# Kernel optimization log

Measured on AMD Instinct MI355X. Metric: run time of the kernel, lower is better.

## Reference

```python
import jax, jax.numpy as jnp
import numpy as np

CS = 128            # config.chunk_size
K = 8               # config.k + 1
EPS = 1e-6          # config.eps
L = K * CS          # extended_len = 1024


def setup_inputs() -> dict:
    key = jax.random.key(0)
    k1, k2 = jax.random.split(key)
    B, T, E = 2, 8192, 256
    x = jax.random.normal(k1, (B, T, E), dtype=jnp.float32)
    # xavier_normal_ on [CS, L]: std = sqrt(2 / (fan_in + fan_out))
    std = np.sqrt(2.0 / (CS + L)).astype(np.float32)
    down_proj = jax.random.normal(k2, (CS, L), dtype=jnp.float32) * std
    return {"x": x, "down_proj": down_proj}


def reference(x, down_proj):
    B, T, E = x.shape
    N = T // CS  # T chosen divisible by CS, so the pad branch is a no-op
    chunks = x.reshape(B, N, CS, E)

    # --- per-chunk retrieval scores (vectorized over the causal chunk loop) ---
    cn = chunks / (jnp.linalg.norm(chunks, axis=-1, keepdims=True) + EPS)
    # row-wise cosine sims between every pair of chunks: [B,N,N,CS,CS]
    sims = jnp.einsum('bice,bjde->bijcd', cn, cn)
    scores = sims.max(axis=-1).sum(axis=-1)              # [B,N,N]
    i_idx = jnp.arange(N)
    causal = i_idx[None, :] < i_idx[:, None]             # j < i allowed
    NEG = jnp.asarray(-1e9, x.dtype)
    scores = jnp.where(causal[None], scores, NEG)

    # --- topk selection, weights (num_sel_i = min(i, K-1)) ---
    vals, idx = jax.lax.top_k(scores, K - 1)             # descending, [B,N,K-1]
    num_sel = jnp.minimum(i_idx, K - 1)                  # [N]
    vmin_slot = jnp.clip(num_sel - 1, 0, K - 2)          # last valid slot = min of topk vals
    v_min = jnp.take_along_axis(vals, jnp.broadcast_to(vmin_slot[None, :, None], (B, N, 1)), axis=-1)
    slot = jnp.arange(K - 1)
    valid = slot[None, :] < num_sel[:, None]             # [N,K-1]
    w = jnp.where(valid[None], vals / (v_min + EPS), 0.0)  # [B,N,K-1]

    # --- weighted gather of selected chunks ---
    b_idx = jnp.arange(B)[:, None, None]
    sel = chunks[b_idx, idx]                             # [B,N,K-1,CS,E]
    weighted = sel * w[..., None, None]

    # --- left-pad to L: zeros occupy leftmost slots, then topk-ordered chunks, then cur ---
    shift = jnp.maximum(0, (K - 1) - i_idx)              # [N]
    src = jnp.clip(slot[None, :] - shift[:, None], 0, K - 2)   # [N,K-1]
    n_idx = jnp.arange(N)[None, :, None]
    arranged = weighted[b_idx, n_idx, src[None]]         # [B,N,K-1,CS,E]
    keep = slot[None, :] >= shift[:, None]
    arranged = jnp.where(keep[None, :, :, None, None], arranged, 0.0)

    ext = jnp.concatenate([arranged.reshape(B, N, (K - 1) * CS, E), chunks], axis=2)  # [B,N,L,E]
    # down_proj @ ext + x_chunks, then contract back to [B,T,E]
    out = jnp.einsum('cl,bnle->bnce', down_proj, ext) + chunks
    return out.reshape(B, N * CS, E)
```

## Files before the change

kernel.cpp:

```cpp
#include <hip/hip_runtime.h>
#include <hip/hip_bf16.h>

#define CS     128
#define EDIM   256
#define NBATCH 2
#define TLEN   8192
#define NCHUNK 64
#define LEXT   1024
#define KSEL   7

typedef __attribute__((ext_vector_type(8))) short   short8;
typedef __attribute__((ext_vector_type(4))) float   floatx4;

__device__ inline short bf16_of(float f) {
    __hip_bfloat16 h = __float2bfloat16(f);
    return *(short*)&h;
}
__device__ inline float f_of_bf16(short s) {
    __hip_bfloat16 h = *(__hip_bfloat16*)&s;
    return __bfloat162float(h);
}

__device__ inline void gl_lds16(const void* g, void* l) {
    __builtin_amdgcn_global_load_lds(
        (const __attribute__((address_space(1))) unsigned int*)g,
        (__attribute__((address_space(3))) unsigned int*)l, 16, 0, 0);
}

#define RAW_BAR() asm volatile("s_barrier" ::: "memory")

__global__ __launch_bounds__(256) void prep_kernel(const float* __restrict__ x,
                                                   const float* __restrict__ dp,
                                                   short* __restrict__ cn_hi,
                                                   short* __restrict__ cn_lo,
                                                   short* __restrict__ xt_hi,
                                                   short* __restrict__ dp_hi) {
    const int bx = blockIdx.x;
    if (bx >= 256) {
        int t = (bx - 256) * 256 + threadIdx.x;
#pragma unroll
        for (int u = 0; u < 16; ++u) {
            int idx = (t * 16 + u) * 4;
            float4 v = *(const float4*)(dp + idx);
            *(short4*)(dp_hi + idx) =
                make_short4(bf16_of(v.x), bf16_of(v.y), bf16_of(v.z), bf16_of(v.w));
        }
        return;
    }

    __shared__ float tile[64 * 257];
    const int b = bx >> 7, t0 = (bx & 127) * 64;
    const int tid = threadIdx.x;
    const int r = tid >> 2, q = tid & 3;

    const float* src = x + ((size_t)(b * TLEN + t0 + r)) * EDIM + q * 64;
    float* trow = &tile[r * 257 + q * 64];
    float s = 0.f;
#pragma unroll
    for (int u = 0; u < 16; ++u) {
        float4 v = *(const float4*)(src + u * 4);
        s += v.x * v.x + v.y * v.y + v.z * v.z + v.w * v.w;
        trow[u * 4 + 0] = v.x; trow[u * 4 + 1] = v.y;
        trow[u * 4 + 2] = v.z; trow[u * 4 + 3] = v.w;
    }
    s += __shfl_xor(s, 1);
    s += __shfl_xor(s, 2);
    const float rn = 1.0f / (sqrtf(s) + 1e-6f);

    short* ch = cn_hi + ((size_t)(b * TLEN + t0 + r)) * EDIM + q * 64;
    short* cl = cn_lo + ((size_t)(b * TLEN + t0 + r)) * EDIM + q * 64;
#pragma unroll
    for (int u = 0; u < 16; ++u) {
        short hs[4], ls[4];
#pragma unroll
        for (int k2 = 0; k2 < 4; ++k2) {
            float c = trow[u * 4 + k2] * rn;
            hs[k2] = bf16_of(c);
            ls[k2] = bf16_of(c - f_of_bf16(hs[k2]));
        }
        *(short4*)(ch + u * 4) = make_short4(hs[0], hs[1], hs[2], hs[3]);
        *(short4*)(cl + u * 4) = make_short4(ls[0], ls[1], ls[2], ls[3]);
    }
    __syncthreads();

    const int g16 = tid >> 4, tq = tid & 15;
#pragma unroll
    for (int it = 0; it < 16; ++it) {
        int e = g16 + it * 16;
        short hs2[4];
#pragma unroll
        for (int g = 0; g < 4; ++g)
            hs2[g] = bf16_of(tile[(tq * 4 + g) * 257 + e]);
        *(short4*)(xt_hi + ((size_t)(b * EDIM + e)) * TLEN + t0 + tq * 4)
            = make_short4(hs2[0], hs2[1], hs2[2], hs2[3]);
    }
}

__global__ __launch_bounds__(512) void scores_mfma(const short* __restrict__ cn_hi,
                                                   const short* __restrict__ cn_lo,
                                                   float* __restrict__ scores) {
    __shared__ short tiles[2][4][4096];
    double* red2   = (double*)&tiles[0][0][0];
    float*  redbuf = (float*)&tiles[0][0][8];

    const int p = blockIdx.x, b = blockIdx.y;
    int i = (int)((1.0f + sqrtf(1.0f + 8.0f * (float)p)) * 0.5f);
    while (i * (i - 1) / 2 > p) --i;
    while (i * (i + 1) / 2 <= p) ++i;
    const int j = p - i * (i - 1) / 2;

    const int tid  = threadIdx.x;
    const int w    = tid >> 6, lane = tid & 63;
    const int wr   = w >> 2, wc = w & 3;
    const int quad = lane >> 4, l15 = lane & 15;

    const int tt = w >> 1, hh = w & 1;
    const short* sarr  = (tt & 1) ? cn_lo : cn_hi;
    const size_t sbase = ((size_t)b * TLEN + ((tt >> 1) ? j : i) * CS) * EDIM;
    const int rr  = lane >> 2;
    const int c16 = (lane & 3) * 8;
    const int csw = c16 ^ (((rr >> 1) & 3) * 8);
    const int q8  = (quad ^ ((l15 >> 1) & 3)) * 8;

    auto stage = [&](int ks, int bf) {
        const short* gsrc = sarr + sbase + ks * 32 + csw;
        short* ldst = &tiles[bf][tt][hh * 2048];
#pragma unroll
        for (int t = 0; t < 4; ++t)
            gl_lds16(gsrc + (size_t)(hh * 64 + 16 * t + rr) * EDIM, ldst + t * 512);
    };

    floatx4 acc[4][2];
#pragma unroll
    for (int rt = 0; rt < 4; ++rt)
#pragma unroll
        for (int ct = 0; ct < 2; ++ct) acc[rt][ct] = (floatx4){0.f, 0.f, 0.f, 0.f};

    stage(0, 0);
    int buf = 0;
    for (int ks = 0; ks < 8; ++ks) {
        if (ks < 7) {
            stage(ks + 1, buf ^ 1);
            asm volatile("s_waitcnt vmcnt(4)" ::: "memory");
        } else {
            asm volatile("s_waitcnt vmcnt(0)" ::: "memory");
        }
        RAW_BAR();

        short8 bh[2], bl[2];
#pragma unroll
        for (int ct = 0; ct < 2; ++ct) {
            int r = wc * 32 + ct * 16 + l15;
            bh[ct] = *(const short8*)&tiles[buf][2][r * 32 + q8];
            bl[ct] = *(const short8*)&tiles[buf][3][r * 32 + q8];
        }
        __builtin_amdgcn_s_setprio(1);
#pragma unroll
        for (int rt = 0; rt < 4; ++rt) {
            int r = wr * 64 + rt * 16 + l15;
            short8 ah = *(const short8*)&tiles[buf][0][r * 32 + q8];
            short8 al = *(const short8*)&tiles[buf][1][r * 32 + q8];
#pragma unroll
            for (int ct = 0; ct < 2; ++ct) {
                acc[rt][ct] = __builtin_amdgcn_mfma_f32_16x16x32_bf16(ah, bh[ct], acc[rt][ct], 0, 0, 0);
                acc[rt][ct] = __builtin_amdgcn_mfma_f32_16x16x32_bf16(ah, bl[ct], acc[rt][ct], 0, 0, 0);
                acc[rt][ct] = __builtin_amdgcn_mfma_f32_16x16x32_bf16(al, bh[ct], acc[rt][ct], 0, 0, 0);
            }
        }
        __builtin_amdgcn_s_setprio(0);
        RAW_BAR();
        buf ^= 1;
    }

#pragma unroll
    for (int rt = 0; rt < 4; ++rt) {
        float m[4];
#pragma unroll
        for (int reg = 0; reg < 4; ++reg)
            m[reg] = fmaxf(acc[rt][0][reg], acc[rt][1][reg]);
#pragma unroll
        for (int off = 1; off < 16; off <<= 1)
#pragma unroll
            for (int reg = 0; reg < 4; ++reg) m[reg] = fmaxf(m[reg], __shfl_xor(m[reg], off));
        if (l15 == 0) {
#pragma unroll
            for (int reg = 0; reg < 4; ++reg)
                redbuf[wc * 128 + wr * 64 + rt * 16 + quad * 4 + reg] = m[reg];
        }
    }
    __syncthreads();

    double part = 0.0;
    if (tid < 128)
        part = (double)fmaxf(fmaxf(redbuf[tid], redbuf[128 + tid]),
                             fmaxf(redbuf[256 + tid], redbuf[384 + tid]));
#pragma unroll
    for (int off = 1; off < 64; off <<= 1) part += __shfl_xor(part, off);
    if (lane == 0 && w < 2) red2[w] = part;
    __syncthreads();
    if (tid == 0) scores[(b * NCHUNK + i) * NCHUNK + j] = (float)(red2[0] + red2[1]);
}

__global__ __launch_bounds__(256) void out_mfma(const float* __restrict__ x,
                                                const short* __restrict__ dph,
                                                const short* __restrict__ xth,
                                                const float* __restrict__ scores,
                                                float* __restrict__ out) {
    __shared__ short As[3][2][128 * 32];
    __shared__ short Bs[3][2][64 * 32];
    __shared__ int   slist[8], sslot[8], snum;
    __shared__ float swei[8];

    const int eq = blockIdx.x, n = blockIdx.y, b = blockIdx.z;
    const int e0 = eq * 64;
    const int tid  = threadIdx.x;
    const int w    = tid >> 6, lane = tid & 63;
    const int wr   = w >> 1, wc = w & 1;
    const int quad = lane >> 4, l15 = lane & 15;
    const int rr   = lane >> 2;
    const int c16  = (lane & 3) * 8;
    const int csw  = c16 ^ (((rr >> 1) & 3) * 8);
    const int q8   = (quad ^ ((l15 >> 1) & 3)) * 8;

    if (w == 0) {
        const float* srow = scores + (b * NCHUNK + n) * NCHUNK;
        const int nsel = n < KSEL ? n : KSEL;
        float v = (lane < n) ? srow[lane] : -3.0e38f;
        float vals[KSEL];
        int   idxs[KSEL];
        for (int s2 = 0; s2 < nsel; ++s2) {
            float bv = v; int bi = lane;
#pragma unroll
            for (int off = 1; off < 64; off <<= 1) {
                float ov = __shfl_xor(bv, off);
                int   oi = __shfl_xor(bi, off);
                if (ov > bv || (ov == bv && oi < bi)) { bv = ov; bi = oi; }
            }
            vals[s2] = bv; idxs[s2] = bi;
            if (lane == bi) v = -3.0e38f;
        }
        if (lane == 0) {
            float vmin = (nsel > 0) ? vals[nsel - 1] : 0.0f;
            float inv  = 1.0f / (vmin + 1e-6f);
            int shift  = KSEL - nsel;
            int c = 0;
            for (int s2 = 0; s2 < 8; ++s2) {
                int jj; float ww;
                if (s2 < KSEL) {
                    int tt = s2 - shift;
                    if (tt >= 0) { jj = idxs[tt]; ww = vals[tt] * inv; }
                    else         { jj = -1;       ww = 0.0f; }
                } else { jj = n; ww = 1.0f; }
                if (jj >= 0) { slist[c] = jj; sslot[c] = s2; swei[c] = ww; ++c; }
            }
            snum = c;
        }
    }
    __syncthreads();
    const int NT = snum * 2;

    auto stage = [&](int st, int b3) {
        int sv = st >> 1, kh = st & 1;
        if (w < 2) {
#pragma unroll
            for (int sub = 0; sub < 2; ++sub) {
                const short* gsrc = dph + (size_t)(sslot[sv] * 128 + (kh * 2 + sub) * 32) + csw;
#pragma unroll
                for (int t = 0; t < 4; ++t)
                    gl_lds16(gsrc + (size_t)(w * 64 + t * 16 + rr) * LEXT,
                             &As[b3][sub][(w * 64 + t * 16) * 32]);
            }
        } else {
#pragma unroll
            for (int sub = 0; sub < 2; ++sub) {
                const short* gsrc = xth + ((size_t)(b * EDIM + e0)) * TLEN
                                    + (size_t)(slist[sv] * CS + (kh * 2 + sub) * 32) + csw;
#pragma unroll
                for (int t = 0; t < 2; ++t)
                    gl_lds16(gsrc + (size_t)((w - 2) * 32 + t * 16 + rr) * TLEN,
                             &Bs[b3][sub][((w - 2) * 32 + t * 16) * 32]);
            }
        }
    };

    floatx4 accT[4][2], accP[4][2];
#pragma unroll
    for (int rt = 0; rt < 4; ++rt)
#pragma unroll
        for (int ct = 0; ct < 2; ++ct) accT[rt][ct] = (floatx4){0.f, 0.f, 0.f, 0.f};

    stage(0, 0);
    if (NT > 1) stage(1, 1);
    if (w < 2) asm volatile("s_waitcnt vmcnt(8)" ::: "memory");
    else       asm volatile("s_waitcnt vmcnt(4)" ::: "memory");

    int cur = 0;
    for (int st = 0; st < NT; ++st) {
        RAW_BAR();

        if ((st & 1) == 0) {
#pragma unroll
            for (int rt = 0; rt < 4; ++rt)
#pragma unroll
                for (int ct = 0; ct < 2; ++ct) accP[rt][ct] = (floatx4){0.f, 0.f, 0.f, 0.f};
        }

#pragma unroll
        for (int sub = 0; sub < 2; ++sub) {
            short8 bh[2];
#pragma unroll
            for (int ct = 0; ct < 2; ++ct) {
                int e = wc * 32 + ct * 16 + l15;
                bh[ct] = *(const short8*)&Bs[cur][sub][e * 32 + q8];
            }
            __builtin_amdgcn_s_setprio(1);
#pragma unroll
            for (int rt = 0; rt < 4; ++rt) {
                int r = wr * 64 + rt * 16 + l15;
                short8 ah = *(const short8*)&As[cur][sub][r * 32 + q8];
#pragma unroll
                for (int ct = 0; ct < 2; ++ct)
                    accP[rt][ct] = __builtin_amdgcn_mfma_f32_16x16x32_bf16(ah, bh[ct], accP[rt][ct], 0, 0, 0);
            }
            __builtin_amdgcn_s_setprio(0);
        }

        if ((st & 1) == 1) {
            float wcur = swei[st >> 1];
#pragma unroll
            for (int rt = 0; rt < 4; ++rt)
#pragma unroll
                for (int ct = 0; ct < 2; ++ct)
#pragma unroll
                    for (int reg = 0; reg < 4; ++reg)
                        accT[rt][ct][reg] += wcur * accP[rt][ct][reg];
        }

        if (st + 2 < NT) {
            int tgt = cur ? cur - 1 : 2;
            stage(st + 2, tgt);
            if (w < 2) asm volatile("s_waitcnt vmcnt(8)" ::: "memory");
            else       asm volatile("s_waitcnt vmcnt(4)" ::: "memory");
        } else if (st + 1 < NT) {
            asm volatile("s_waitcnt vmcnt(0)" ::: "memory");
        }
        cur = (cur == 2) ? 0 : cur + 1;
    }

#pragma unroll
    for (int rt = 0; rt < 4; ++rt)
#pragma unroll
        for (int ct = 0; ct < 2; ++ct) {
#pragma unroll
            for (int reg = 0; reg < 4; ++reg) {
                int row = wr * 64 + rt * 16 + quad * 4 + reg;
                int col = wc * 32 + ct * 16 + l15;
                size_t o = ((size_t)(b * TLEN + n * CS + row)) * EDIM + e0 + col;
                out[o] = accT[rt][ct][reg] + x[o];
            }
        }
}

extern "C" void kernel_launch(void* const* d_in, const int* in_sizes, int n_in,
                              void* d_out, int out_size, void* d_ws, size_t ws_size,
                              hipStream_t stream) {
    const float* x  = (const float*)d_in[0];
    const float* dp = (const float*)d_in[1];
    float* out = (float*)d_out;

    char* ws = (char*)d_ws;
    short* cn_hi  = (short*)(ws);
    short* cn_lo  = (short*)(ws + (8u << 20));
    short* xt_hi  = (short*)(ws + (16u << 20));
    short* dp_hi  = (short*)(ws + (24u << 20));
    float* scores = (float*)(ws + (25u << 20));

    prep_kernel <<<dim3(264), 256, 0, stream>>>(x, dp, cn_hi, cn_lo, xt_hi, dp_hi);
    scores_mfma <<<dim3(NCHUNK * (NCHUNK - 1) / 2, NBATCH), 512, 0, stream>>>(cn_hi, cn_lo, scores);
    out_mfma    <<<dim3(4, NCHUNK, NBATCH), 256, 0, stream>>>(x, dp_hi, xt_hi, scores, out);
}
```

Baseline: 203.9 us.

## Compute 2x2 chunk-pair blocks per scores workgroup to reuse loaded tiles

The scores kernel now processes a 2x2 block of chunk pairs (i in {2I,2I+1}, j in {2J,2J+1}) per workgroup over a triangular grid of 32x33/2 blocks. Each staged chunk tile is reused across two pairs, which halves global/LDS loads per pair, and each wave now holds a 64x128 accumulator tile. Diagonal blocks compute some non-causal pairs that are then discarded. Costs include higher register pressure (32 accumulators per wave), doubled LDS (64KB) and fewer workgroups.

```diff
diff --git a/kernel.cpp b/kernel.cpp
--- a/kernel.cpp
+++ b/kernel.cpp
@@ -96,27 +96,28 @@
     }
 }
 
-__global__ __launch_bounds__(512) void scores_mfma(const short* __restrict__ cn_hi,
-                                                   const short* __restrict__ cn_lo,
-                                                   float* __restrict__ scores) {
-    __shared__ short tiles[2][4][4096];
-    double* red2   = (double*)&tiles[0][0][0];
-    float*  redbuf = (float*)&tiles[0][0][8];
+__global__ __launch_bounds__(512, 2) void scores_mfma(const short* __restrict__ cn_hi,
+                                                      const short* __restrict__ cn_lo,
+                                                      float* __restrict__ scores) {
+    __shared__ short tiles[2][4][2][4096];
+    double* red2   = (double*)&tiles[0][0][0][0];
+    float*  redbuf = (float*)((char*)&tiles[0][0][0][0] + 64);
 
     const int p = blockIdx.x, b = blockIdx.y;
-    int i = (int)((1.0f + sqrtf(1.0f + 8.0f * (float)p)) * 0.5f);
-    while (i * (i - 1) / 2 > p) --i;
-    while (i * (i + 1) / 2 <= p) ++i;
-    const int j = p - i * (i - 1) / 2;
+    int I = (int)((sqrtf(8.0f * (float)p + 1.0f) - 1.0f) * 0.5f);
+    while (I * (I + 1) / 2 > p) --I;
+    while ((I + 1) * (I + 2) / 2 <= p) ++I;
+    const int J = p - I * (I + 1) / 2;
 
     const int tid  = threadIdx.x;
     const int w    = tid >> 6, lane = tid & 63;
-    const int wr   = w >> 2, wc = w & 3;
+    const int pr   = w >> 1, h = w & 1;
     const int quad = lane >> 4, l15 = lane & 15;
 
-    const int tt = w >> 1, hh = w & 1;
-    const short* sarr  = (tt & 1) ? cn_lo : cn_hi;
-    const size_t sbase = ((size_t)b * TLEN + ((tt >> 1) ? j : i) * CS) * EDIM;
+    const int c_stage = w >> 1, hl = w & 1;
+    const int chunk_c = (c_stage < 2) ? (2 * I + c_stage) : (2 * J + (c_stage - 2));
+    const short* sarr  = hl ? cn_lo : cn_hi;
+    const size_t sbase = ((size_t)b * TLEN + (size_t)chunk_c * CS) * EDIM;
     const int rr  = lane >> 2;
     const int c16 = (lane & 3) * 8;
     const int csw = c16 ^ (((rr >> 1) & 3) * 8);
@@ -124,47 +125,50 @@
 
     auto stage = [&](int ks, int bf) {
         const short* gsrc = sarr + sbase + ks * 32 + csw;
-        short* ldst = &tiles[bf][tt][hh * 2048];
-#pragma unroll
-        for (int t = 0; t < 4; ++t)
-            gl_lds16(gsrc + (size_t)(hh * 64 + 16 * t + rr) * EDIM, ldst + t * 512);
+        short* ldst = &tiles[bf][c_stage][hl][0];
+#pragma unroll
+        for (int t = 0; t < 8; ++t)
+            gl_lds16(gsrc + (size_t)(16 * t + rr) * EDIM, ldst + t * 512);
     };
 
-    floatx4 acc[4][2];
+    const int ci = pr >> 1;
+    const int cj = 2 + (pr & 1);
+
+    floatx4 acc[4][8];
 #pragma unroll
     for (int rt = 0; rt < 4; ++rt)
 #pragma unroll
-        for (int ct = 0; ct < 2; ++ct) acc[rt][ct] = (floatx4){0.f, 0.f, 0.f, 0.f};
+        for (int ct = 0; ct < 8; ++ct) acc[rt][ct] = (floatx4){0.f, 0.f, 0.f, 0.f};
 
     stage(0, 0);
     int buf = 0;
     for (int ks = 0; ks < 8; ++ks) {
         if (ks < 7) {
             stage(ks + 1, buf ^ 1);
-            asm volatile("s_waitcnt vmcnt(4)" ::: "memory");
+            asm volatile("s_waitcnt vmcnt(8)" ::: "memory");
         } else {
             asm volatile("s_waitcnt vmcnt(0)" ::: "memory");
         }
         RAW_BAR();
 
-        short8 bh[2], bl[2];
-#pragma unroll
-        for (int ct = 0; ct < 2; ++ct) {
-            int r = wc * 32 + ct * 16 + l15;
-            bh[ct] = *(const short8*)&tiles[buf][2][r * 32 + q8];
-            bl[ct] = *(const short8*)&tiles[buf][3][r * 32 + q8];
+        short8 ah[4], al[4];
+#pragma unroll
+        for (int rt = 0; rt < 4; ++rt) {
+            int r = h * 64 + rt * 16 + l15;
+            ah[rt] = *(const short8*)&tiles[buf][ci][0][r * 32 + q8];
+            al[rt] = *(const short8*)&tiles[buf][ci][1][r * 32 + q8];
         }
         __builtin_amdgcn_s_setprio(1);
 #pragma unroll
-        for (int rt = 0; rt < 4; ++rt) {
-            int r = wr * 64 + rt * 16 + l15;
-            short8 ah = *(const short8*)&tiles[buf][0][r * 32 + q8];
-            short8 al = *(const short8*)&tiles[buf][1][r * 32 + q8];
-#pragma unroll
-            for (int ct = 0; ct < 2; ++ct) {
-                acc[rt][ct] = __builtin_amdgcn_mfma_f32_16x16x32_bf16(ah, bh[ct], acc[rt][ct], 0, 0, 0);
-                acc[rt][ct] = __builtin_amdgcn_mfma_f32_16x16x32_bf16(ah, bl[ct], acc[rt][ct], 0, 0, 0);
-                acc[rt][ct] = __builtin_amdgcn_mfma_f32_16x16x32_bf16(al, bh[ct], acc[rt][ct], 0, 0, 0);
+        for (int ct = 0; ct < 8; ++ct) {
+            int r = ct * 16 + l15;
+            short8 bh = *(const short8*)&tiles[buf][cj][0][r * 32 + q8];
+            short8 bl = *(const short8*)&tiles[buf][cj][1][r * 32 + q8];
+#pragma unroll
+            for (int rt = 0; rt < 4; ++rt) {
+                acc[rt][ct] = __builtin_amdgcn_mfma_f32_16x16x32_bf16(ah[rt], bh, acc[rt][ct], 0, 0, 0);
+                acc[rt][ct] = __builtin_amdgcn_mfma_f32_16x16x32_bf16(ah[rt], bl, acc[rt][ct], 0, 0, 0);
+                acc[rt][ct] = __builtin_amdgcn_mfma_f32_16x16x32_bf16(al[rt], bh, acc[rt][ct], 0, 0, 0);
             }
         }
         __builtin_amdgcn_s_setprio(0);
@@ -172,12 +176,18 @@
         buf ^= 1;
     }
 
+    __syncthreads();
+
 #pragma unroll
     for (int rt = 0; rt < 4; ++rt) {
         float m[4];
 #pragma unroll
-        for (int reg = 0; reg < 4; ++reg)
-            m[reg] = fmaxf(acc[rt][0][reg], acc[rt][1][reg]);
+        for (int reg = 0; reg < 4; ++reg) {
+            float mm = acc[rt][0][reg];
+#pragma unroll
+            for (int ct = 1; ct < 8; ++ct) mm = fmaxf(mm, acc[rt][ct][reg]);
+            m[reg] = mm;
+        }
 #pragma unroll
         for (int off = 1; off < 16; off <<= 1)
 #pragma unroll
@@ -185,20 +195,27 @@
         if (l15 == 0) {
 #pragma unroll
             for (int reg = 0; reg < 4; ++reg)
-                redbuf[wc * 128 + wr * 64 + rt * 16 + quad * 4 + reg] = m[reg];
-        }
-    }
-    __syncthreads();
-
-    double part = 0.0;
-    if (tid < 128)
-        part = (double)fmaxf(fmaxf(redbuf[tid], redbuf[128 + tid]),
-                             fmaxf(redbuf[256 + tid], redbuf[384 + tid]));
-#pragma unroll
-    for (int off = 1; off < 64; off <<= 1) part += __shfl_xor(part, off);
-    if (lane == 0 && w < 2) red2[w] = part;
-    __syncthreads();
-    if (tid == 0) scores[(b * NCHUNK + i) * NCHUNK + j] = (float)(red2[0] + red2[1]);
+                redbuf[pr * 128 + h * 64 + rt * 16 + quad * 4 + reg] = m[reg];
+        }
+    }
+    __syncthreads();
+
+    {
+        const int tp = tid >> 7, row = tid & 127;
+        double part = (double)redbuf[tp * 128 + row];
+#pragma unroll
+        for (int off = 1; off < 64; off <<= 1) part += __shfl_xor(part, off);
+        if (lane == 0) red2[w] = part;
+    }
+    __syncthreads();
+    if (tid < 4) {
+        const int a = tid >> 1, bs = tid & 1;
+        const int i_g = 2 * I + a, j_g = 2 * J + bs;
+        if (j_g < i_g) {
+            double sum = red2[2 * tid] + red2[2 * tid + 1];
+            scores[(b * NCHUNK + i_g) * NCHUNK + j_g] = (float)sum;
+        }
+    }
 }
 
 __global__ __launch_bounds__(256) void out_mfma(const float* __restrict__ x,
@@ -376,6 +393,6 @@
     float* scores = (float*)(ws + (25u << 20));
 
     prep_kernel <<<dim3(264), 256, 0, stream>>>(x, dp, cn_hi, cn_lo, xt_hi, dp_hi);
-    scores_mfma <<<dim3(NCHUNK * (NCHUNK - 1) / 2, NBATCH), 512, 0, stream>>>(cn_hi, cn_lo, scores);
+    scores_mfma <<<dim3(32 * 33 / 2, NBATCH), 512, 0, stream>>>(cn_hi, cn_lo, scores);
     out_mfma    <<<dim3(4, NCHUNK, NBATCH), 256, 0, stream>>>(x, dp_hi, xt_hi, scores, out);
 }
```

Result: no change. 205.8 us (+0.9%).

## Repack xt and down_proj into k-blocked layouts and halve scores block size

Applied to the files above, without the earlier changes.

The prep kernel now writes the transposed bf16 x and the bf16 down_proj in a k-tiled layout of contiguous 32-element rows per 128- or 256-row slab. The out kernel's global-to-LDS loads then read 64-byte contiguous rows instead of rows strided by TLEN or LEXT, which is meant to improve DRAM and TLB locality. Separately, the scores kernel drops from 8 to 4 waves per block. Each wave stages one full 128-row operand tile and computes a 64x64 output tile, which raises per-thread register use and changes occupancy.

```diff
diff --git a/kernel.cpp b/kernel.cpp
--- a/kernel.cpp
+++ b/kernel.cpp
@@ -33,8 +33,8 @@
                                                    const float* __restrict__ dp,
                                                    short* __restrict__ cn_hi,
                                                    short* __restrict__ cn_lo,
-                                                   short* __restrict__ xt_hi,
-                                                   short* __restrict__ dp_hi) {
+                                                   short* __restrict__ xkt,
+                                                   short* __restrict__ dpk) {
     const int bx = blockIdx.x;
     if (bx >= 256) {
         int t = (bx - 256) * 256 + threadIdx.x;
@@ -42,7 +42,10 @@
         for (int u = 0; u < 16; ++u) {
             int idx = (t * 16 + u) * 4;
             float4 v = *(const float4*)(dp + idx);
-            *(short4*)(dp_hi + idx) =
+            int c = idx >> 10, l = idx & 1023;
+            int s = l >> 7, kk = (l >> 5) & 3, kq = l & 31;
+            int na = ((s * 4 + kk) * 128 + c) * 32 + kq;
+            *(short4*)(dpk + na) =
                 make_short4(bf16_of(v.x), bf16_of(v.y), bf16_of(v.z), bf16_of(v.w));
         }
         return;
@@ -84,6 +87,10 @@
     __syncthreads();
 
     const int g16 = tid >> 4, tq = tid & 15;
+    const int chunk = t0 >> 7;
+    const int kbase = (t0 & 64) + tq * 4;
+    const int kk = kbase >> 5, kq = kbase & 31;
+    short* xbase = xkt + ((size_t)(((b * 64 + chunk) * 4 + kk) * 256)) * 32 + kq;
 #pragma unroll
     for (int it = 0; it < 16; ++it) {
         int e = g16 + it * 16;
@@ -91,12 +98,11 @@
 #pragma unroll
         for (int g = 0; g < 4; ++g)
             hs2[g] = bf16_of(tile[(tq * 4 + g) * 257 + e]);
-        *(short4*)(xt_hi + ((size_t)(b * EDIM + e)) * TLEN + t0 + tq * 4)
-            = make_short4(hs2[0], hs2[1], hs2[2], hs2[3]);
-    }
-}
-
-__global__ __launch_bounds__(512) void scores_mfma(const short* __restrict__ cn_hi,
+        *(short4*)(xbase + (size_t)e * 32) = make_short4(hs2[0], hs2[1], hs2[2], hs2[3]);
+    }
+}
+
+__global__ __launch_bounds__(256) void scores_mfma(const short* __restrict__ cn_hi,
                                                    const short* __restrict__ cn_lo,
                                                    float* __restrict__ scores) {
     __shared__ short tiles[2][4][4096];
@@ -111,12 +117,11 @@
 
     const int tid  = threadIdx.x;
     const int w    = tid >> 6, lane = tid & 63;
-    const int wr   = w >> 2, wc = w & 3;
+    const int wr   = w >> 1, wc = w & 1;
     const int quad = lane >> 4, l15 = lane & 15;
 
-    const int tt = w >> 1, hh = w & 1;
-    const short* sarr  = (tt & 1) ? cn_lo : cn_hi;
-    const size_t sbase = ((size_t)b * TLEN + ((tt >> 1) ? j : i) * CS) * EDIM;
+    const short* sarr  = (w & 1) ? cn_lo : cn_hi;
+    const size_t sbase = ((size_t)b * TLEN + ((w >> 1) ? j : i) * CS) * EDIM;
     const int rr  = lane >> 2;
     const int c16 = (lane & 3) * 8;
     const int csw = c16 ^ (((rr >> 1) & 3) * 8);
@@ -124,33 +129,33 @@
 
     auto stage = [&](int ks, int bf) {
         const short* gsrc = sarr + sbase + ks * 32 + csw;
-        short* ldst = &tiles[bf][tt][hh * 2048];
-#pragma unroll
-        for (int t = 0; t < 4; ++t)
-            gl_lds16(gsrc + (size_t)(hh * 64 + 16 * t + rr) * EDIM, ldst + t * 512);
+        short* ldst = &tiles[bf][w][0];
+#pragma unroll
+        for (int t = 0; t < 8; ++t)
+            gl_lds16(gsrc + (size_t)(16 * t + rr) * EDIM, ldst + t * 512);
     };
 
-    floatx4 acc[4][2];
+    floatx4 acc[4][4];
 #pragma unroll
     for (int rt = 0; rt < 4; ++rt)
 #pragma unroll
-        for (int ct = 0; ct < 2; ++ct) acc[rt][ct] = (floatx4){0.f, 0.f, 0.f, 0.f};
+        for (int ct = 0; ct < 4; ++ct) acc[rt][ct] = (floatx4){0.f, 0.f, 0.f, 0.f};
 
     stage(0, 0);
     int buf = 0;
     for (int ks = 0; ks < 8; ++ks) {
         if (ks < 7) {
             stage(ks + 1, buf ^ 1);
-            asm volatile("s_waitcnt vmcnt(4)" ::: "memory");
+            asm volatile("s_waitcnt vmcnt(8)" ::: "memory");
         } else {
             asm volatile("s_waitcnt vmcnt(0)" ::: "memory");
         }
         RAW_BAR();
 
-        short8 bh[2], bl[2];
-#pragma unroll
-        for (int ct = 0; ct < 2; ++ct) {
-            int r = wc * 32 + ct * 16 + l15;
+        short8 bh[4], bl[4];
+#pragma unroll
+        for (int ct = 0; ct < 4; ++ct) {
+            int r = wc * 64 + ct * 16 + l15;
             bh[ct] = *(const short8*)&tiles[buf][2][r * 32 + q8];
             bl[ct] = *(const short8*)&tiles[buf][3][r * 32 + q8];
         }
@@ -161,7 +166,7 @@
             short8 ah = *(const short8*)&tiles[buf][0][r * 32 + q8];
             short8 al = *(const short8*)&tiles[buf][1][r * 32 + q8];
 #pragma unroll
-            for (int ct = 0; ct < 2; ++ct) {
+            for (int ct = 0; ct < 4; ++ct) {
                 acc[rt][ct] = __builtin_amdgcn_mfma_f32_16x16x32_bf16(ah, bh[ct], acc[rt][ct], 0, 0, 0);
                 acc[rt][ct] = __builtin_amdgcn_mfma_f32_16x16x32_bf16(ah, bl[ct], acc[rt][ct], 0, 0, 0);
                 acc[rt][ct] = __builtin_amdgcn_mfma_f32_16x16x32_bf16(al, bh[ct], acc[rt][ct], 0, 0, 0);
@@ -176,8 +181,12 @@
     for (int rt = 0; rt < 4; ++rt) {
         float m[4];
 #pragma unroll
-        for (int reg = 0; reg < 4; ++reg)
-            m[reg] = fmaxf(acc[rt][0][reg], acc[rt][1][reg]);
+        for (int reg = 0; reg < 4; ++reg) {
+            float mm = acc[rt][0][reg];
+#pragma unroll
+            for (int ct = 1; ct < 4; ++ct) mm = fmaxf(mm, acc[rt][ct][reg]);
+            m[reg] = mm;
+        }
 #pragma unroll
         for (int off = 1; off < 16; off <<= 1)
 #pragma unroll
@@ -191,9 +200,7 @@
     __syncthreads();
 
     double part = 0.0;
-    if (tid < 128)
-        part = (double)fmaxf(fmaxf(redbuf[tid], redbuf[128 + tid]),
-                             fmaxf(redbuf[256 + tid], redbuf[384 + tid]));
+    if (tid < 128) part = (double)fmaxf(redbuf[tid], redbuf[128 + tid]);
 #pragma unroll
     for (int off = 1; off < 64; off <<= 1) part += __shfl_xor(part, off);
     if (lane == 0 && w < 2) red2[w] = part;
@@ -202,8 +209,8 @@
 }
 
 __global__ __launch_bounds__(256) void out_mfma(const float* __restrict__ x,
-                                                const short* __restrict__ dph,
-                                                const short* __restrict__ xth,
+                                                const short* __restrict__ dpk,
+                                                const short* __restrict__ xkt,
                                                 const float* __restrict__ scores,
                                                 float* __restrict__ out) {
     __shared__ short As[3][2][128 * 32];
@@ -264,20 +271,21 @@
         if (w < 2) {
 #pragma unroll
             for (int sub = 0; sub < 2; ++sub) {
-                const short* gsrc = dph + (size_t)(sslot[sv] * 128 + (kh * 2 + sub) * 32) + csw;
+                const short* gsrc = dpk
+                    + (size_t)((sslot[sv] * 4 + kh * 2 + sub) * 128) * 32 + csw;
 #pragma unroll
                 for (int t = 0; t < 4; ++t)
-                    gl_lds16(gsrc + (size_t)(w * 64 + t * 16 + rr) * LEXT,
+                    gl_lds16(gsrc + (size_t)(w * 64 + t * 16 + rr) * 32,
                              &As[b3][sub][(w * 64 + t * 16) * 32]);
             }
         } else {
 #pragma unroll
             for (int sub = 0; sub < 2; ++sub) {
-                const short* gsrc = xth + ((size_t)(b * EDIM + e0)) * TLEN
-                                    + (size_t)(slist[sv] * CS + (kh * 2 + sub) * 32) + csw;
+                const short* gsrc = xkt
+                    + (size_t)((((b * 64 + slist[sv]) * 4 + kh * 2 + sub) * 256) + e0) * 32 + csw;
 #pragma unroll
                 for (int t = 0; t < 2; ++t)
-                    gl_lds16(gsrc + (size_t)((w - 2) * 32 + t * 16 + rr) * TLEN,
+                    gl_lds16(gsrc + (size_t)((w - 2) * 32 + t * 16 + rr) * 32,
                              &Bs[b3][sub][((w - 2) * 32 + t * 16) * 32]);
             }
         }
@@ -371,11 +379,11 @@
     char* ws = (char*)d_ws;
     short* cn_hi  = (short*)(ws);
     short* cn_lo  = (short*)(ws + (8u << 20));
-    short* xt_hi  = (short*)(ws + (16u << 20));
-    short* dp_hi  = (short*)(ws + (24u << 20));
+    short* xkt    = (short*)(ws + (16u << 20));
+    short* dpk    = (short*)(ws + (24u << 20));
     float* scores = (float*)(ws + (25u << 20));
 
-    prep_kernel <<<dim3(264), 256, 0, stream>>>(x, dp, cn_hi, cn_lo, xt_hi, dp_hi);
-    scores_mfma <<<dim3(NCHUNK * (NCHUNK - 1) / 2, NBATCH), 512, 0, stream>>>(cn_hi, cn_lo, scores);
-    out_mfma    <<<dim3(4, NCHUNK, NBATCH), 256, 0, stream>>>(x, dp_hi, xt_hi, scores, out);
-}
+    prep_kernel <<<dim3(264), 256, 0, stream>>>(x, dp, cn_hi, cn_lo, xkt, dpk);
+    scores_mfma <<<dim3(NCHUNK * (NCHUNK - 1) / 2, NBATCH), 256, 0, stream>>>(cn_hi, cn_lo, scores);
+    out_mfma    <<<dim3(4, NCHUNK, NBATCH), 256, 0, stream>>>(x, dpk, xkt, scores, out);
+}
```

New measurement: 200.0 us. About the same (-1.9%).
